# Performance work log

Hardware: AMD Instinct MI355X
Metric: run time of the kernel (lower is better)

## Reference

```python
import jax, jax.numpy as jnp
import numpy as np

jax.config.update("jax_enable_x64", True)

N_QUBITS = 21
N_LAYERS = 2
N_PARAMS = (N_LAYERS + 1) * N_QUBITS  # 63

# CNOT in |ctrl,tgt> basis, reshaped to (c_out, t_out, c_in, t_in)
_CNOT = jnp.array([[1, 0, 0, 0],
                   [0, 1, 0, 0],
                   [0, 0, 0, 1],
                   [0, 0, 1, 0]], dtype=jnp.complex128).reshape(2, 2, 2, 2)


def _ry(theta):
    # RY(theta) = [[cos(t/2), -sin(t/2)], [sin(t/2), cos(t/2)]]
    c = jnp.cos(theta * 0.5).astype(jnp.complex128)
    s = jnp.sin(theta * 0.5).astype(jnp.complex128)
    return jnp.stack([jnp.stack([c, -s]), jnp.stack([s, c])])


def _apply_1q(state, gate, q):
    # Contract 2x2 gate into qubit axis q of the (2,)*n state tensor.
    state = jnp.tensordot(gate, state, axes=((1,), (q,)))
    return jnp.moveaxis(state, 0, q)


def _apply_cnot(state, q):
    # CNOT with control q, target q+1 (qubit 0 = most-significant axis).
    state = jnp.tensordot(_CNOT, state, axes=((2, 3), (q, q + 1)))
    return jnp.moveaxis(state, (0, 1), (q, q + 1))


def setup_inputs() -> dict:
    key = jax.random.key(0)
    params = jax.random.uniform(key, (N_PARAMS,), dtype=jnp.float32) * (2.0 * np.pi)
    return {"params": params}


def reference(params):
    p = params.astype(jnp.float64)
    # |0...0> as a (2,)*n tensor
    state = jnp.zeros((2,) * N_QUBITS, dtype=jnp.complex128)
    state = state.at[(0,) * N_QUBITS].set(1.0 + 0.0j)
    idx = 0
    for _ in range(N_LAYERS):
        for q in range(N_QUBITS):
            state = _apply_1q(state, _ry(p[idx]), q)
            idx += 1
        for q in range(N_QUBITS - 1):
            state = _apply_cnot(state, q)
    for q in range(N_QUBITS):
        state = _apply_1q(state, _ry(p[idx]), q)
        idx += 1
    state = state.reshape(-1)  # (2**N_QUBITS,)
    return state / jnp.linalg.norm(state)
```

## Files before the change

kernel.cpp:

```cpp
#include <hip/hip_runtime.h>


#define NQ 21
#define NSTATE (1 << NQ)
#define SW(t) ((t) + ((t) >> 5))

typedef float f32x4 __attribute__((ext_vector_type(4)));

template <int BIT, int N>
__device__ __forceinline__ void ry_bf(float (&v)[N], float c, float s) {
#pragma unroll
  for (int m = 0; m < N; ++m)
    if ((m & (1 << BIT)) == 0) {
      float a = v[m], b = v[m | (1 << BIT)];
      v[m] = c * a - s * b;
      v[m | (1 << BIT)] = s * a + c * b;
    }
}

template <int CBIT, int TBIT, int N>
__device__ __forceinline__ void cnot_rr(float (&v)[N]) {
#pragma unroll
  for (int m = 0; m < N; ++m)
    if ((m & (1 << CBIT)) && !(m & (1 << TBIT))) {
      float t = v[m];
      v[m] = v[m | (1 << TBIT)];
      v[m | (1 << TBIT)] = t;
    }
}

__global__ __launch_bounds__(256, 4) void fused(const float* __restrict__ p,
                                                float* __restrict__ out,
                                                int outmode) {
  __shared__ float2 csn[63];
  __shared__ float ex[2][2112];
  const int tid = threadIdx.x;
  const int bid = blockIdx.x;
  if (tid < 63) {
    float h = 0.5f * p[tid];
    csn[tid] = float2{cosf(h), sinf(h)};
  }
  __syncthreads();

  float W[2][2];
  {
    const int b0 = (bid >> 9) & 1;
    const float2 g30 = csn[42], g20 = csn[21], g10 = csn[0];
    const float r00 = b0 ? g30.y : g30.x;
    const float r01 = b0 ? g30.x : -g30.y;
    float w00 = r00 * g20.x * g10.x;
    float w01 = r00 * (-g20.y) * g10.y;
    float w10 = r01 * g20.y * g10.x;
    float w11 = r01 * g20.x * g10.y;
#pragma unroll
    for (int q = 1; q <= 9; ++q) {
      const int bq = (bid >> (9 - q)) & 1;
      const float2 g1 = csn[q], g2 = csn[21 + q], g3 = csn[42 + q];
      const float c1 = g1.x, s1 = g1.y;
      const float c2 = g2.x, s2 = g2.y;
      const float c3 = g3.x, s3 = g3.y;
      const float h00 = c1 * w00 + s1 * w01;
      const float h01 = c1 * w10 + s1 * w11;
      const float h10 = s1 * w00 + c1 * w01;
      const float h11 = s1 * w10 + c1 * w11;
      const float m00 = c2 * h00 + s2 * h01;
      const float m01 = s2 * h00 + c2 * h01;
      const float m10 = -s2 * h10 + c2 * h11;
      const float m11 = c2 * h10 - s2 * h11;
      const float r0 = bq ? s3 : c3;
      const float r1 = bq ? c3 : -s3;
      w00 = r0 * m00;
      w01 = r0 * m10;
      w10 = r1 * m01;
      w11 = r1 * m11;
    }
    const float2 g1b = csn[10], g2b = csn[31], gW = csn[11];
    const float hh00 = g1b.x * w00 + g1b.y * w01;
    const float hh01 = g1b.x * w10 + g1b.y * w11;
    const float hh10 = g1b.y * w00 + g1b.x * w01;
    const float hh11 = g1b.y * w10 + g1b.x * w11;
    const float a00 = g2b.x * hh00 + g2b.y * hh01;
    const float a10 = g2b.y * hh00 + g2b.x * hh01;
    const float a01 = -g2b.y * hh10 + g2b.x * hh11;
    const float a11 = g2b.x * hh10 - g2b.y * hh11;
    W[0][0] = a00 * gW.x + a01 * gW.y;
    W[0][1] = a00 * gW.y + a01 * gW.x;
    W[1][0] = a10 * gW.x + a11 * gW.y;
    W[1][1] = a10 * gW.y + a11 * gW.x;
  }

  float v[8];
  {
    const int gt = tid ^ (tid >> 1);
    float tcommon = 1.0f;
#pragma unroll
    for (int b = 0; b < 7; ++b) {
      const float2 gb = csn[20 - b];
      tcommon *= ((gt >> b) & 1) ? gb.y : gb.x;
    }
    const int t7 = (tid >> 7) & 1;
    const float2 g13 = csn[13], g12 = csn[12];
    const float s13_0 = t7 ? g13.y : g13.x;
    const float s13_1 = t7 ? g13.x : g13.y;
#pragma unroll
    for (int r = 0; r < 8; ++r) {
      const int gr = r ^ (r >> 1);
      float prod = tcommon * W[(r >> 2) & 1][(r >> 1) & 1];
      prod *= (r & 1) ? s13_1 : s13_0;
      prod *= (gr & 1) ? g12.y : g12.x;
      v[r] = prod;
    }
  }

  ry_bf<1>(v, csn[32].x, csn[32].y);
  ry_bf<0>(v, csn[33].x, csn[33].y);
  cnot_rr<2, 1>(v);
  cnot_rr<1, 0>(v);
  ry_bf<2>(v, csn[52].x, csn[52].y);
  ry_bf<1>(v, csn[53].x, csn[53].y);

#pragma unroll
  for (int r = 0; r < 8; ++r) ex[0][SW((r << 8) | tid)] = v[r];
  __syncthreads();
#pragma unroll
  for (int r = 0; r < 8; ++r)
    v[r] = ex[0][SW(((tid >> 6) << 9) | (r << 6) | (tid & 63))];

  ry_bf<1>(v, csn[34].x, csn[34].y);
  ry_bf<0>(v, csn[35].x, csn[35].y);
  cnot_rr<2, 1>(v);
  cnot_rr<1, 0>(v);
  ry_bf<2>(v, csn[54].x, csn[54].y);
  ry_bf<1>(v, csn[55].x, csn[55].y);

#pragma unroll
  for (int r = 0; r < 8; ++r)
    ex[1][SW(((tid >> 6) << 9) | (r << 6) | (tid & 63))] = v[r];
  __syncthreads();
#pragma unroll
  for (int r = 0; r < 8; ++r)
    v[r] = ex[1][SW(((tid >> 4) << 7) | (r << 4) | (tid & 15))];

  ry_bf<1>(v, csn[36].x, csn[36].y);
  ry_bf<0>(v, csn[37].x, csn[37].y);
  cnot_rr<2, 1>(v);
  cnot_rr<1, 0>(v);
  ry_bf<2>(v, csn[56].x, csn[56].y);
  ry_bf<1>(v, csn[57].x, csn[57].y);

#pragma unroll
  for (int r = 0; r < 8; ++r)
    ex[0][SW(((tid >> 4) << 7) | (r << 4) | (tid & 15))] = v[r];
  __syncthreads();
#pragma unroll
  for (int r = 0; r < 8; ++r)
    v[r] = ex[0][SW(((tid >> 2) << 5) | (r << 2) | (tid & 3))];

  ry_bf<1>(v, csn[38].x, csn[38].y);
  ry_bf<0>(v, csn[39].x, csn[39].y);
  cnot_rr<2, 1>(v);
  cnot_rr<1, 0>(v);
  ry_bf<2>(v, csn[58].x, csn[58].y);
  ry_bf<1>(v, csn[59].x, csn[59].y);

#pragma unroll
  for (int r = 0; r < 8; ++r)
    ex[1][SW(((tid >> 2) << 5) | (r << 2) | (tid & 3))] = v[r];
  __syncthreads();
#pragma unroll
  for (int r = 0; r < 8; ++r) v[r] = ex[1][SW((tid << 3) | r)];

  ry_bf<1>(v, csn[40].x, csn[40].y);
  ry_bf<0>(v, csn[41].x, csn[41].y);
  cnot_rr<2, 1>(v);
  cnot_rr<1, 0>(v);
  ry_bf<2>(v, csn[60].x, csn[60].y);
  ry_bf<1>(v, csn[61].x, csn[61].y);
  ry_bf<0>(v, csn[62].x, csn[62].y);

  const int base = (bid << 11) | (tid << 3);
  if (outmode == 2) {
    f32x4* o4 = (f32x4*)out;
#pragma unroll
    for (int i = 0; i < 4; ++i) {
      f32x4 w = {v[2 * i], 0.0f, v[2 * i + 1], 0.0f};
      __builtin_nontemporal_store(w, &o4[(base >> 1) + i]);
    }
  } else {
    f32x4* o4 = (f32x4*)(out + base);
#pragma unroll
    for (int j = 0; j < 2; ++j) {
      f32x4 w = {v[4 * j], v[4 * j + 1], v[4 * j + 2], v[4 * j + 3]};
      __builtin_nontemporal_store(w, &o4[j]);
    }
  }
}

extern "C" void kernel_launch(void* const* d_in, const int* in_sizes, int n_in,
                              void* d_out, int out_size, void* d_ws,
                              size_t ws_size, hipStream_t stream) {
  const float* p = (const float*)d_in[0];
  float* out = (float*)d_out;
  const int outmode = (out_size == 2 * NSTATE) ? 2 : 1;
  fused<<<1024, 256, 0, stream>>>(p, out, outmode);
}
```

Before: 59.88 us.

## Replace shared-memory transposes with wave-level shuffles over per-wave slabs

After: 62.33 us. 4.1% more time.

```diff
diff --git a/kernel.cpp b/kernel.cpp
--- a/kernel.cpp
+++ b/kernel.cpp
@@ -3,9 +3,8 @@
 
 #define NQ 21
 #define NSTATE (1 << NQ)
-#define SW(t) ((t) + ((t) >> 5))
 
-typedef float f32x4 __attribute__((ext_vector_type(4)));
+typedef float f32x2 __attribute__((ext_vector_type(2)));
 
 template <int BIT, int N>
 __device__ __forceinline__ void ry_bf(float (&v)[N], float c, float s) {
@@ -29,22 +28,44 @@
     }
 }
 
+template <int MASK, int N>
+__device__ __forceinline__ void ry_shfl(float (&u)[N], float c, float s,
+                                        int lane) {
+  const float ss = (lane & MASK) ? s : -s;
+#pragma unroll
+  for (int e = 0; e < N; ++e) {
+    float w = __shfl_xor(u[e], MASK);
+    u[e] = c * u[e] + ss * w;
+  }
+}
+
+template <int CMASK, int TMASK, int N>
+__device__ __forceinline__ void cnot_shfl(float (&u)[N], int lane) {
+  const bool ctrl = (lane & CMASK) != 0;
+#pragma unroll
+  for (int e = 0; e < N; ++e) {
+    float w = __shfl_xor(u[e], TMASK);
+    u[e] = ctrl ? w : u[e];
+  }
+}
+
 __global__ __launch_bounds__(256, 4) void fused(const float* __restrict__ p,
                                                 float* __restrict__ out,
                                                 int outmode) {
   __shared__ float2 csn[63];
-  __shared__ float ex[2][2112];
   const int tid = threadIdx.x;
-  const int bid = blockIdx.x;
   if (tid < 63) {
     float h = 0.5f * p[tid];
     csn[tid] = float2{cosf(h), sinf(h)};
   }
   __syncthreads();
 
+  const int lane = tid & 63;
+  const int slab = (blockIdx.x << 2) | (tid >> 6);
+
   float W[2][2];
   {
-    const int b0 = (bid >> 9) & 1;
+    const int b0 = (slab >> 11) & 1;
     const float2 g30 = csn[42], g20 = csn[21], g10 = csn[0];
     const float r00 = b0 ? g30.y : g30.x;
     const float r01 = b0 ? g30.x : -g30.y;
@@ -53,8 +74,8 @@
     float w10 = r01 * g20.y * g10.x;
     float w11 = r01 * g20.x * g10.y;
 #pragma unroll
-    for (int q = 1; q <= 9; ++q) {
-      const int bq = (bid >> (9 - q)) & 1;
+    for (int q = 1; q <= 11; ++q) {
+      const int bq = (slab >> (11 - q)) & 1;
       const float2 g1 = csn[q], g2 = csn[21 + q], g3 = csn[42 + q];
       const float c1 = g1.x, s1 = g1.y;
       const float c2 = g2.x, s2 = g2.y;
@@ -74,7 +95,7 @@
       w10 = r1 * m01;
       w11 = r1 * m11;
     }
-    const float2 g1b = csn[10], g2b = csn[31], gW = csn[11];
+    const float2 g1b = csn[12], g2b = csn[33], gW = csn[13];
     const float hh00 = g1b.x * w00 + g1b.y * w01;
     const float hh01 = g1b.x * w10 + g1b.y * w11;
     const float hh10 = g1b.y * w00 + g1b.x * w01;
@@ -91,108 +112,67 @@
 
   float v[8];
   {
-    const int gt = tid ^ (tid >> 1);
-    float tcommon = 1.0f;
+    const int gl = lane ^ (lane >> 1);
+    float tlane = 1.0f;
 #pragma unroll
-    for (int b = 0; b < 7; ++b) {
+    for (int b = 0; b < 5; ++b) {
       const float2 gb = csn[20 - b];
-      tcommon *= ((gt >> b) & 1) ? gb.y : gb.x;
+      tlane *= ((gl >> b) & 1) ? gb.y : gb.x;
     }
-    const int t7 = (tid >> 7) & 1;
-    const float2 g13 = csn[13], g12 = csn[12];
-    const float s13_0 = t7 ? g13.y : g13.x;
-    const float s13_1 = t7 ? g13.x : g13.y;
+    const int x5 = (lane >> 5) & 1;
+    const float2 g15 = csn[15], g14 = csn[14];
+    const float s15_0 = x5 ? g15.y : g15.x;
+    const float s15_1 = x5 ? g15.x : g15.y;
 #pragma unroll
     for (int r = 0; r < 8; ++r) {
-      const int gr = r ^ (r >> 1);
-      float prod = tcommon * W[(r >> 2) & 1][(r >> 1) & 1];
-      prod *= (r & 1) ? s13_1 : s13_0;
-      prod *= (gr & 1) ? g12.y : g12.x;
+      float prod = tlane * W[(r >> 2) & 1][(r >> 1) & 1];
+      prod *= (r & 1) ? s15_1 : s15_0;
+      prod *= ((r ^ (r >> 1)) & 1) ? g14.y : g14.x;
       v[r] = prod;
     }
   }
 
-  ry_bf<1>(v, csn[32].x, csn[32].y);
-  ry_bf<0>(v, csn[33].x, csn[33].y);
+  ry_bf<1>(v, csn[34].x, csn[34].y);
+  ry_bf<0>(v, csn[35].x, csn[35].y);
+  ry_shfl<32>(v, csn[36].x, csn[36].y, lane);
+  ry_shfl<16>(v, csn[37].x, csn[37].y, lane);
+  ry_shfl<8>(v, csn[38].x, csn[38].y, lane);
+  ry_shfl<4>(v, csn[39].x, csn[39].y, lane);
+  ry_shfl<2>(v, csn[40].x, csn[40].y, lane);
+  ry_shfl<1>(v, csn[41].x, csn[41].y, lane);
   cnot_rr<2, 1>(v);
   cnot_rr<1, 0>(v);
-  ry_bf<2>(v, csn[52].x, csn[52].y);
-  ry_bf<1>(v, csn[53].x, csn[53].y);
-
-#pragma unroll
-  for (int r = 0; r < 8; ++r) ex[0][SW((r << 8) | tid)] = v[r];
-  __syncthreads();
-#pragma unroll
-  for (int r = 0; r < 8; ++r)
-    v[r] = ex[0][SW(((tid >> 6) << 9) | (r << 6) | (tid & 63))];
-
-  ry_bf<1>(v, csn[34].x, csn[34].y);
-  ry_bf<0>(v, csn[35].x, csn[35].y);
-  cnot_rr<2, 1>(v);
-  cnot_rr<1, 0>(v);
+  v[1] = __shfl_xor(v[1], 32);
+  v[3] = __shfl_xor(v[3], 32);
+  v[5] = __shfl_xor(v[5], 32);
+  v[7] = __shfl_xor(v[7], 32);
+  cnot_shfl<32, 16>(v, lane);
+  cnot_shfl<16, 8>(v, lane);
+  cnot_shfl<8, 4>(v, lane);
+  cnot_shfl<4, 2>(v, lane);
+  cnot_shfl<2, 1>(v, lane);
   ry_bf<2>(v, csn[54].x, csn[54].y);
   ry_bf<1>(v, csn[55].x, csn[55].y);
+  ry_bf<0>(v, csn[56].x, csn[56].y);
+  ry_shfl<32>(v, csn[57].x, csn[57].y, lane);
+  ry_shfl<16>(v, csn[58].x, csn[58].y, lane);
+  ry_shfl<8>(v, csn[59].x, csn[59].y, lane);
+  ry_shfl<4>(v, csn[60].x, csn[60].y, lane);
+  ry_shfl<2>(v, csn[61].x, csn[61].y, lane);
+  ry_shfl<1>(v, csn[62].x, csn[62].y, lane);
 
+  const int base = (slab << 9) | lane;
+  if (outmode == 2) {
+    f32x2* o2 = (f32x2*)out;
 #pragma unroll
-  for (int r = 0; r < 8; ++r)
-    ex[1][SW(((tid >> 6) << 9) | (r << 6) | (tid & 63))] = v[r];
-  __syncthreads();
-#pragma unroll
-  for (int r = 0; r < 8; ++r)
-    v[r] = ex[1][SW(((tid >> 4) << 7) | (r << 4) | (tid & 15))];
-
-  ry_bf<1>(v, csn[36].x, csn[36].y);
-  ry_bf<0>(v, csn[37].x, csn[37].y);
-  cnot_rr<2, 1>(v);
-  cnot_rr<1, 0>(v);
-  ry_bf<2>(v, csn[56].x, csn[56].y);
-  ry_bf<1>(v, csn[57].x, csn[57].y);
-
-#pragma unroll
-  for (int r = 0; r < 8; ++r)
-    ex[0][SW(((tid >> 4) << 7) | (r << 4) | (tid & 15))] = v[r];
-  __syncthreads();
-#pragma unroll
-  for (int r = 0; r < 8; ++r)
-    v[r] = ex[0][SW(((tid >> 2) << 5) | (r << 2) | (tid & 3))];
-
-  ry_bf<1>(v, csn[38].x, csn[38].y);
-  ry_bf<0>(v, csn[39].x, csn[39].y);
-  cnot_rr<2, 1>(v);
-  cnot_rr<1, 0>(v);
-  ry_bf<2>(v, csn[58].x, csn[58].y);
-  ry_bf<1>(v, csn[59].x, csn[59].y);
-
-#pragma unroll
-  for (int r = 0; r < 8; ++r)
-    ex[1][SW(((tid >> 2) << 5) | (r << 2) | (tid & 3))] = v[r];
-  __syncthreads();
-#pragma unroll
-  for (int r = 0; r < 8; ++r) v[r] = ex[1][SW((tid << 3) | r)];
-
-  ry_bf<1>(v, csn[40].x, csn[40].y);
-  ry_bf<0>(v, csn[41].x, csn[41].y);
-  cnot_rr<2, 1>(v);
-  cnot_rr<1, 0>(v);
-  ry_bf<2>(v, csn[60].x, csn[60].y);
-  ry_bf<1>(v, csn[61].x, csn[61].y);
-  ry_bf<0>(v, csn[62].x, csn[62].y);
-
-  const int base = (bid << 11) | (tid << 3);
-  if (outmode == 2) {
-    f32x4* o4 = (f32x4*)out;
-#pragma unroll
-    for (int i = 0; i < 4; ++i) {
-      f32x4 w = {v[2 * i], 0.0f, v[2 * i + 1], 0.0f};
-      __builtin_nontemporal_store(w, &o4[(base >> 1) + i]);
+    for (int r = 0; r < 8; ++r) {
+      f32x2 w = {v[r], 0.0f};
+      __builtin_nontemporal_store(w, &o2[base + (r << 6)]);
     }
   } else {
-    f32x4* o4 = (f32x4*)(out + base);
 #pragma unroll
-    for (int j = 0; j < 2; ++j) {
-      f32x4 w = {v[4 * j], v[4 * j + 1], v[4 * j + 2], v[4 * j + 3]};
-      __builtin_nontemporal_store(w, &o4[j]);
-    }
+    for (int r = 0; r < 8; ++r)
+      __builtin_nontemporal_store(v[r], &out[base + (r << 6)]);
   }
 }
 
```
